# Kernel optimization log

Measured on AMD Instinct MI355X. Metric: run time of the kernel, lower is better.

Reference implementation:

```python
import jax, jax.numpy as jnp
import numpy as np


def setup_inputs() -> dict:
    key = jax.random.key(0)
    ks = jax.random.split(key, 12)
    B, L, N, C, Ct, H, RH1, RH2, S = 64, 64, 256, 8, 4, 128, 128, 64, 4
    def rn(k, shape, s=0.08):
        return jax.random.normal(k, shape, dtype=jnp.float32) * s
    return dict(
        x=jax.random.normal(ks[0], (B, L, N, C * Ct), dtype=jnp.float32),
        hidden_intensity=jax.random.normal(ks[1], (B, N, H), dtype=jnp.float32),
        r=jax.random.normal(ks[2], (B, S), dtype=jnp.float32),
        W_ih=rn(ks[3], (4 * H, C)), W_hh=rn(ks[4], (4 * H, H)),
        b_ih=jnp.zeros((4 * H,), jnp.float32), b_hh=jnp.zeros((4 * H,), jnp.float32),
        W1=rn(ks[5], (RH1, 2 * H + 1)), b1=jnp.zeros((RH1,), jnp.float32),
        W2=rn(ks[6], (RH2, RH1)), b2=jnp.zeros((RH2,), jnp.float32),
        W3=rn(ks[7], (C, RH2)), b3=jnp.zeros((C,), jnp.float32),
        Wf=rn(ks[8], (1, C)), bf=jnp.zeros((1,), jnp.float32),
    )


def reference(x, hidden_intensity, r, W_ih, W_hh, b_ih, b_hh,
              W1, b1, W2, b2, W3, b3, Wf, bf):
    # Faithful to torch: nn.LSTM has batch_first=False but is fed (B, L, C),
    # so B is the sequence axis, L the batch axis, and lstm_out[:, -1, :]
    # writes predictions into that last column, so only x[:, -1] matters.
    B, L, N, _ = x.shape
    C = W_ih.shape[1]
    Ct = x.shape[3] // C
    H = W_hh.shape[1]

    def lstm_all_times(seq):  # seq: (T, Bb, C) -> hidden at every time (T, Bb, H)
        xp = jnp.einsum('tbc,gc->tbg', seq, W_ih) + b_ih + b_hh  # (T, Bb, 4H)
        def step(carry, xt):
            h, c = carry
            g = xt + h @ W_hh.T
            i, f, gg, o = jnp.split(g, 4, axis=-1)  # torch gate order i,f,g,o
            c = jax.nn.sigmoid(f) * c + jax.nn.sigmoid(i) * jnp.tanh(gg)
            h = jax.nn.sigmoid(o) * jnp.tanh(c)
            return (h, c), h
        z0 = jnp.zeros((seq.shape[1], H), seq.dtype)
        _, hs = jax.lax.scan(step, (z0, z0), xp)
        return hs

    hi = jnp.broadcast_to(hidden_intensity[:, :, None, :], (B, N, Ct, H))

    def roll(last_col, rj):  # last_col: (B, N, Ct, C), rj: (B,)
        hs = lstm_all_times(last_col.reshape(B, N * Ct, C)).reshape(B, N, Ct, H)
        rr = jnp.broadcast_to(rj[:, None, None, None], (B, N, Ct, 1))
        z = jnp.concatenate([hs, hi, rr], axis=-1)       # (B, N, Ct, 2H+1)
        h1 = jax.nn.relu(z @ W1.T + b1)
        h2 = jax.nn.relu(h1 @ W2.T + b2)
        pr = h2 @ W3.T + b3                              # (B, N, Ct, C)
        contrib = (jax.nn.relu(pr) @ Wf.T + bf)[..., 0].sum(axis=2)  # (B, N)
        return pr, contrib

    last0 = x[:, -1, :, :].reshape(B, N, Ct, C)
    _, preds = jax.lax.scan(roll, last0, r.T)  # (S, B, N)
    return jnp.transpose(preds, (1, 2, 0))     # (B, N, steps_ahead)
```

## Files before the change

### kernel.cpp

```cpp
#include <hip/hip_runtime.h>
#include <hip/hip_bf16.h>


typedef __attribute__((ext_vector_type(8))) _Float16 half8;
typedef __attribute__((ext_vector_type(4))) float f32x4;

#define MFMAH(a, b, c) __builtin_amdgcn_mfma_f32_16x16x32_f16(a, b, c, 0, 0, 0)

__device__ __forceinline__ float sigf(float x)   { return 1.0f / (1.0f + __expf(-x)); }
__device__ __forceinline__ float tanh_f(float x) { return 1.0f - 2.0f / (__expf(2.0f * x) + 1.0f); }

__global__ void prep_k(const float* __restrict__ x, const float* __restrict__ hi,
                       const float* __restrict__ W1, const float* __restrict__ W2,
                       const float* __restrict__ W3, const float* __restrict__ W_hh,
                       const float* __restrict__ W_ih,
                       _Float16* __restrict__ cur16, _Float16* __restrict__ hi16,
                       _Float16* __restrict__ wp1, _Float16* __restrict__ wp2,
                       _Float16* __restrict__ wp3, _Float16* __restrict__ wpB)
{
    int i = blockIdx.x * 256 + threadIdx.x;
    if (i < 524288) {
        int b = i >> 13, rem = i & 8191;
        cur16[i] = (_Float16)x[(size_t)b * 524288 + 63 * 8192 + rem];
        return;
    }
    i -= 524288;
    if (i < 2097152) { hi16[i] = (_Float16)hi[i]; return; }
    i -= 2097152;
    if (i < 32768) {
        int fragid = i >> 9, lj = i & 511;
        int kt = fragid >> 3, nt = fragid & 7;
        int l = lj >> 3, j = lj & 7;
        int k = kt * 32 + (l >> 4) * 8 + j;
        int o = nt * 16 + (l & 15);
        wp1[i] = (_Float16)W1[o * 257 + k];
        return;
    }
    i -= 32768;
    if (i < 8192) {
        int fragid = i >> 9, lj = i & 511;
        int kt = fragid >> 2, nt = fragid & 3;
        int l = lj >> 3, j = lj & 7;
        int k = kt * 32 + (l >> 4) * 8 + j;
        int o = nt * 16 + (l & 15);
        wp2[i] = (_Float16)W2[o * 128 + k];
        return;
    }
    i -= 8192;
    if (i < 1024) {
        int kt = i >> 9, lj = i & 511;
        int l = lj >> 3, j = lj & 7;
        int k = kt * 32 + (l >> 4) * 8 + j;
        int c = l & 15;
        wp3[i] = (_Float16)((c < 8) ? W3[c * 64 + k] : 0.0f);
        return;
    }
    i -= 1024;
    if (i < 81920) {
        int frag = i >> 9, lj = i & 511;
        int kt = frag >> 5, ntile = frag & 31;
        int l = lj >> 3, j = lj & 7;
        int klocal = (l >> 4) * 8 + j;
        int col = ntile * 16 + (l & 15);
        float v;
        if (kt < 4) v = W_hh[col * 128 + kt * 32 + klocal];
        else        v = (klocal < 8) ? W_ih[col * 8 + klocal] : 0.0f;
        wpB[i] = (_Float16)v;
    }
}

__global__ __launch_bounds__(512, 2) void lstm_mfma_k(
    const _Float16* __restrict__ cur16, const _Float16* __restrict__ wpB,
    const float* __restrict__ b_ih, const float* __restrict__ b_hh,
    _Float16* __restrict__ hs16)
{
    __shared__ __align__(16) _Float16 zone[2][4][640];
    __shared__ __align__(16) _Float16 xz[64][32];

    const int t  = threadIdx.x;
    const int cg = t >> 6, l = t & 63;
    const int li = l & 15, lk = l >> 4;
    const int q0 = blockIdx.x * 4;

    half8 bw[4][5];
#pragma unroll
    for (int g = 0; g < 4; ++g)
#pragma unroll
        for (int kt = 0; kt < 5; ++kt) {
            bw[g][kt] = *(const half8*)(wpB + (size_t)(kt * 32 + g * 8 + cg) * 512 + l * 8);
            asm volatile("" : "+a"(bw[g][kt]));
        }

    f32x4 bs4[4];
#pragma unroll
    for (int g = 0; g < 4; ++g) {
        int gc = g * 128 + cg * 16 + li;
        float bv = b_ih[gc] + b_hh[gc];
        bs4[g] = (f32x4){bv, bv, bv, bv};
    }

    for (int i = t; i < 1280; i += 512) ((uint*)zone)[i] = 0;
    if (t < 256) {
        int step = t >> 2, tt = t & 3;
        *(uint4*)&xz[step][tt * 8] =
            *(const uint4*)(cur16 + (size_t)step * 8192 + q0 * 8 + tt * 8);
    }
    float cc = 0.0f;
    __syncthreads();

    const int zpl   = cg >> 1;
    const int jl    = (cg & 1) * 16 + li;
    const int roff  = (li & 12) * 40 + lk * 8;
    const int srow  = lk * 4;

    _Float16* ph = hs16 + (size_t)(q0 + lk) * 128 + cg * 16 + li;
    const _Float16* xrd = &xz[0][(li >> 2) * 8];

    f32x4 accx[4];
    {
        half8 xa0 = *(const half8*)(xrd);
#pragma unroll
        for (int g = 0; g < 4; ++g)
            accx[g] = MFMAH(xa0, bw[g][4], bs4[g]);
    }

    auto dostep = [&](int step, int p) {
        const int pn = p ^ 1;

        half8 ah[4];
#pragma unroll
        for (int kt = 0; kt < 4; ++kt)
            ah[kt] = *(const half8*)&zone[p][kt][roff];

        const f32x4 z4 = (f32x4){0.0f, 0.0f, 0.0f, 0.0f};
        f32x4 a0[4], a1[4];
#pragma unroll
        for (int g = 0; g < 4; ++g) {
            a0[g] = MFMAH(ah[0], bw[g][0], accx[g]);
            a1[g] = MFMAH(ah[2], bw[g][2], z4);
        }
#pragma unroll
        for (int g = 0; g < 4; ++g) {
            a0[g] = MFMAH(ah[1], bw[g][1], a0[g]);
            a1[g] = MFMAH(ah[3], bw[g][3], a1[g]);
        }

        float pi = a0[0][0] + a1[0][0];
        float pf = a0[1][0] + a1[1][0];
        float pg = a0[2][0] + a1[2][0];
        float po = a0[3][0] + a1[3][0];
        cc = sigf(pf) * cc + sigf(pi) * tanh_f(pg);
        float hv = sigf(po) * tanh_f(cc);
        _Float16 h16 = (_Float16)hv;
        zone[pn][zpl][srow * 40 + jl] = h16;
        ph[(size_t)step * 131072] = h16;
        asm volatile("s_waitcnt lgkmcnt(0)\n\ts_barrier" ::: "memory");

        half8 xn = *(const half8*)(xrd + ((step + 1) & 63) * 32);
#pragma unroll
        for (int g = 0; g < 4; ++g)
            accx[g] = MFMAH(xn, bw[g][4], bs4[g]);
    };

    for (int s2 = 0; s2 < 32; ++s2) {
        dostep(s2 * 2,     0);
        dostep(s2 * 2 + 1, 1);
    }
}

__global__ __launch_bounds__(256, 3) void mlp_mfma_k(
    const _Float16* __restrict__ hs16, const _Float16* __restrict__ hi16,
    const float* __restrict__ r, int jstep,
    const _Float16* __restrict__ wp1, const _Float16* __restrict__ wp2,
    const _Float16* __restrict__ wp3,
    const float* __restrict__ W1, const float* __restrict__ b1,
    const float* __restrict__ b2, const float* __restrict__ b3,
    const float* __restrict__ Wf, const float* __restrict__ bfp,
    _Float16* __restrict__ cur16, float* __restrict__ out)
{
    __shared__ __align__(16) _Float16 h1f[4 * 4 * 640];
    __shared__ __align__(16) _Float16 h2f[2 * 4 * 640];

    const int t = threadIdx.x;
    const int w = t >> 6, l = t & 63;
    const int lrow = l & 15, lk = l >> 4;
    const int b = blockIdx.x >> 4;
    const int qb = (blockIdx.x & 15) * 64;
    const float rb = r[b * 4 + jstep];

    f32x4 acc[4][2];
#pragma unroll
    for (int nt = 0; nt < 2; ++nt) {
        int col = w * 32 + nt * 16 + lrow;
        float bias = b1[col] + rb * W1[col * 257 + 256];
#pragma unroll
        for (int mt = 0; mt < 4; ++mt)
            acc[mt][nt] = (f32x4){bias, bias, bias, bias};
    }

#pragma unroll 4
    for (int kt = 0; kt < 8; ++kt) {
        half8 av[4];
#pragma unroll
        for (int mt = 0; mt < 4; ++mt) {
            int q = qb + mt * 16 + lrow;
            if (kt < 4) {
                av[mt] = *(const half8*)(hs16 + (size_t)(b * 1024 + q) * 128
                                          + kt * 32 + lk * 8);
            } else {
                av[mt] = *(const half8*)(hi16 + (size_t)(b * 256 + (q >> 2)) * 128
                                          + (kt - 4) * 32 + lk * 8);
            }
        }
#pragma unroll
        for (int nt = 0; nt < 2; ++nt) {
            half8 bv = *(const half8*)(wp1 + (size_t)(kt * 8 + w * 2 + nt) * 512 + l * 8);
#pragma unroll
            for (int mt = 0; mt < 4; ++mt)
                acc[mt][nt] = MFMAH(av[mt], bv, acc[mt][nt]);
        }
    }

#pragma unroll
    for (int mt = 0; mt < 4; ++mt)
#pragma unroll
        for (int nt = 0; nt < 2; ++nt)
#pragma unroll
            for (int reg = 0; reg < 4; ++reg) {
                float v = fmaxf(acc[mt][nt][reg], 0.0f);
                int s = lk * 4 + reg, jj = nt * 16 + lrow;
                h1f[(w * 4 + mt) * 640 + s * 40 + jj] = (_Float16)v;
            }
    __syncthreads();

    f32x4 acc2[4];
    {
        float bias = b2[16 * w + lrow];
#pragma unroll
        for (int mt = 0; mt < 4; ++mt)
            acc2[mt] = (f32x4){bias, bias, bias, bias};
    }
#pragma unroll
    for (int kt = 0; kt < 4; ++kt) {
        half8 bv = *(const half8*)(wp2 + (size_t)(kt * 4 + w) * 512 + l * 8);
#pragma unroll
        for (int mt = 0; mt < 4; ++mt) {
            half8 a = *(const half8*)&h1f[(kt * 4 + mt) * 640 + lrow * 40 + lk * 8];
            acc2[mt] = MFMAH(a, bv, acc2[mt]);
        }
    }
#pragma unroll
    for (int mt = 0; mt < 4; ++mt)
#pragma unroll
        for (int reg = 0; reg < 4; ++reg) {
            float v = fmaxf(acc2[mt][reg], 0.0f);
            int s = lk * 4 + reg, jl2 = (w & 1) * 16 + lrow;
            h2f[((w >> 1) * 4 + mt) * 640 + s * 40 + jl2] = (_Float16)v;
        }
    __syncthreads();

    f32x4 acc3 = (f32x4){0.0f, 0.0f, 0.0f, 0.0f};
#pragma unroll
    for (int kt = 0; kt < 2; ++kt) {
        half8 a  = *(const half8*)&h2f[(kt * 4 + w) * 640 + lrow * 40 + lk * 8];
        half8 bv = *(const half8*)(wp3 + (size_t)kt * 512 + l * 8);
        acc3 = MFMAH(a, bv, acc3);
    }

    const int c = lrow;
    const float b3v = (c < 8) ? b3[c] : 0.0f;
    const float wfv = (c < 8) ? Wf[c] : 0.0f;
    float fr[4];
#pragma unroll
    for (int reg = 0; reg < 4; ++reg) {
        float pr = acc3[reg] + b3v;
        if (c < 8) {
            int row = 16 * w + lk * 4 + reg;
            cur16[((size_t)(b * 1024 + qb + row)) * 8 + c] = (_Float16)pr;
        }
        fr[reg] = (c < 8) ? fmaxf(pr, 0.0f) * wfv : 0.0f;
    }
#pragma unroll
    for (int reg = 0; reg < 4; ++reg) {
        fr[reg] += __shfl_xor(fr[reg], 1);
        fr[reg] += __shfl_xor(fr[reg], 2);
        fr[reg] += __shfl_xor(fr[reg], 4);
    }
    if ((l & 15) == 0) {
        int n = (qb + 16 * w + lk * 4) >> 2;
        float v = fr[0] + fr[1] + fr[2] + fr[3] + 4.0f * bfp[0];
        out[(size_t)(b * 256 + n) * 4 + jstep] = v;
    }
}

extern "C" void kernel_launch(void* const* d_in, const int* in_sizes, int n_in,
                              void* d_out, int out_size, void* d_ws, size_t ws_size,
                              hipStream_t stream)
{
    const float* x   = (const float*)d_in[0];
    const float* hi  = (const float*)d_in[1];
    const float* r   = (const float*)d_in[2];
    const float* Wih = (const float*)d_in[3];
    const float* Whh = (const float*)d_in[4];
    const float* bih = (const float*)d_in[5];
    const float* bhh = (const float*)d_in[6];
    const float* W1  = (const float*)d_in[7];
    const float* b1  = (const float*)d_in[8];
    const float* W2  = (const float*)d_in[9];
    const float* b2  = (const float*)d_in[10];
    const float* W3  = (const float*)d_in[11];
    const float* b3  = (const float*)d_in[12];
    const float* Wf  = (const float*)d_in[13];
    const float* bf  = (const float*)d_in[14];
    float* out = (float*)d_out;

    _Float16* cur16 = (_Float16*)d_ws;
    _Float16* hs16  = cur16 + 524288;
    _Float16* hi16  = hs16 + 8388608;
    _Float16* wp1   = hi16 + 2097152;
    _Float16* wp2   = wp1 + 32768;
    _Float16* wp3   = wp2 + 8192;
    _Float16* wpB   = wp3 + 1024;

    prep_k<<<10724, 256, 0, stream>>>(x, hi, W1, W2, W3, Whh, Wih,
                                      cur16, hi16, wp1, wp2, wp3, wpB);
    for (int j = 0; j < 4; ++j) {
        lstm_mfma_k<<<256, 512, 0, stream>>>(cur16, wpB, bih, bhh, hs16);
        mlp_mfma_k<<<1024, 256, 0, stream>>>(hs16, hi16, r, j, wp1, wp2, wp3,
                                             W1, b1, b2, b3, Wf, bf, cur16, out);
    }
}
```

Measured before the change: 286.7 us.

## Vectorize prep conversions, reorder LSTM gates with setprio, double-buffer MLP A loads

Result: faster. 279.3 us (-2.6%).

```diff
diff --git a/kernel.cpp b/kernel.cpp
--- a/kernel.cpp
+++ b/kernel.cpp
@@ -19,14 +19,26 @@
                        _Float16* __restrict__ wp3, _Float16* __restrict__ wpB)
 {
     int i = blockIdx.x * 256 + threadIdx.x;
-    if (i < 524288) {
-        int b = i >> 13, rem = i & 8191;
-        cur16[i] = (_Float16)x[(size_t)b * 524288 + 63 * 8192 + rem];
-        return;
-    }
-    i -= 524288;
-    if (i < 2097152) { hi16[i] = (_Float16)hi[i]; return; }
-    i -= 2097152;
+    if (i < 65536) {
+        int e = i * 8;
+        int b = e >> 13, rem = e & 8191;
+        const float* src = x + (size_t)b * 524288 + 63 * 8192 + rem;
+        half8 v;
+#pragma unroll
+        for (int k = 0; k < 8; ++k) v[k] = (_Float16)src[k];
+        *(half8*)(cur16 + e) = v;
+        return;
+    }
+    i -= 65536;
+    if (i < 262144) {
+        int e = i * 8;
+        half8 v;
+#pragma unroll
+        for (int k = 0; k < 8; ++k) v[k] = (_Float16)hi[e + k];
+        *(half8*)(hi16 + e) = v;
+        return;
+    }
+    i -= 262144;
     if (i < 32768) {
         int fragid = i >> 9, lj = i & 511;
         int kt = fragid >> 3, nt = fragid & 7;
@@ -82,19 +94,20 @@
     const int li = l & 15, lk = l >> 4;
     const int q0 = blockIdx.x * 4;
 
+    const int gsrc[4] = {1, 0, 2, 3};
     half8 bw[4][5];
 #pragma unroll
     for (int g = 0; g < 4; ++g)
 #pragma unroll
         for (int kt = 0; kt < 5; ++kt) {
-            bw[g][kt] = *(const half8*)(wpB + (size_t)(kt * 32 + g * 8 + cg) * 512 + l * 8);
+            bw[g][kt] = *(const half8*)(wpB + (size_t)(kt * 32 + gsrc[g] * 8 + cg) * 512 + l * 8);
             asm volatile("" : "+a"(bw[g][kt]));
         }
 
     f32x4 bs4[4];
 #pragma unroll
     for (int g = 0; g < 4; ++g) {
-        int gc = g * 128 + cg * 16 + li;
+        int gc = gsrc[g] * 128 + cg * 16 + li;
         float bv = b_ih[gc] + b_hh[gc];
         bs4[g] = (f32x4){bv, bv, bv, bv};
     }
@@ -132,6 +145,7 @@
         for (int kt = 0; kt < 4; ++kt)
             ah[kt] = *(const half8*)&zone[p][kt][roff];
 
+        __builtin_amdgcn_s_setprio(1);
         const f32x4 z4 = (f32x4){0.0f, 0.0f, 0.0f, 0.0f};
         f32x4 a0[4], a1[4];
 #pragma unroll
@@ -145,12 +159,14 @@
             a1[g] = MFMAH(ah[3], bw[g][3], a1[g]);
         }
 
-        float pi = a0[0][0] + a1[0][0];
-        float pf = a0[1][0] + a1[1][0];
+        float pf = a0[0][0] + a1[0][0];
+        float sf = sigf(pf);
+        float pi = a0[1][0] + a1[1][0];
         float pg = a0[2][0] + a1[2][0];
         float po = a0[3][0] + a1[3][0];
-        cc = sigf(pf) * cc + sigf(pi) * tanh_f(pg);
+        cc = sf * cc + sigf(pi) * tanh_f(pg);
         float hv = sigf(po) * tanh_f(cc);
+        __builtin_amdgcn_s_setprio(0);
         _Float16 h16 = (_Float16)hv;
         zone[pn][zpl][srow * 40 + jl] = h16;
         ph[(size_t)step * 131072] = h16;
@@ -198,26 +214,32 @@
             acc[mt][nt] = (f32x4){bias, bias, bias, bias};
     }
 
-#pragma unroll 4
-    for (int kt = 0; kt < 8; ++kt) {
-        half8 av[4];
+    auto loadA = [&](int kt, half8* av) {
 #pragma unroll
         for (int mt = 0; mt < 4; ++mt) {
             int q = qb + mt * 16 + lrow;
-            if (kt < 4) {
+            if (kt < 4)
                 av[mt] = *(const half8*)(hs16 + (size_t)(b * 1024 + q) * 128
                                           + kt * 32 + lk * 8);
-            } else {
+            else
                 av[mt] = *(const half8*)(hi16 + (size_t)(b * 256 + (q >> 2)) * 128
                                           + (kt - 4) * 32 + lk * 8);
-            }
-        }
+        }
+    };
+
+    half8 avA[4], avB[4];
+    loadA(0, avA);
+#pragma unroll
+    for (int kt = 0; kt < 8; ++kt) {
+        half8* cur = (kt & 1) ? avB : avA;
+        half8* nxt = (kt & 1) ? avA : avB;
+        if (kt < 7) loadA(kt + 1, nxt);
 #pragma unroll
         for (int nt = 0; nt < 2; ++nt) {
             half8 bv = *(const half8*)(wp1 + (size_t)(kt * 8 + w * 2 + nt) * 512 + l * 8);
 #pragma unroll
             for (int mt = 0; mt < 4; ++mt)
-                acc[mt][nt] = MFMAH(av[mt], bv, acc[mt][nt]);
+                acc[mt][nt] = MFMAH(cur[mt], bv, acc[mt][nt]);
         }
     }
 
@@ -322,8 +344,8 @@
     _Float16* wp3   = wp2 + 8192;
     _Float16* wpB   = wp3 + 1024;
 
-    prep_k<<<10724, 256, 0, stream>>>(x, hi, W1, W2, W3, Whh, Wih,
-                                      cur16, hi16, wp1, wp2, wp3, wpB);
+    prep_k<<<1764, 256, 0, stream>>>(x, hi, W1, W2, W3, Whh, Wih,
+                                     cur16, hi16, wp1, wp2, wp3, wpB);
     for (int j = 0; j < 4; ++j) {
         lstm_mfma_k<<<256, 512, 0, stream>>>(cur16, wpB, bih, bhh, hs16);
         mlp_mfma_k<<<1024, 256, 0, stream>>>(hs16, hi16, r, j, wp1, wp2, wp3,
```
